# Kernel optimization log

Hardware: AMD Instinct MI355X
Metric: run time of the kernel (lower is better)

## Reference

```python
import jax, jax.numpy as jnp
import numpy as np

GAMMA = 0.1      # L1 weight
N_STEPS = 10     # inner ISTA/RMSProp iterations
RHO = 0.9        # RMSProp decay
LR = 0.001
MOMENTUM = 0.9
EPS = 1e-8       # RMSProp epsilon
ABS_EPS = 1e-6   # smooth-abs epsilon (seya diff_abs)


def setup_inputs() -> dict:
    key = jax.random.key(0)
    k1, k2 = jax.random.split(key)
    B, D_in, D_out = 32768, 128, 512
    inputs = jax.random.normal(k1, (B, D_in), dtype=jnp.float32)
    # glorot_uniform for W of shape (output_dim, input_dim)
    limit = float(np.sqrt(6.0 / (D_out + D_in)))
    W = jax.random.uniform(k2, (D_out, D_in), jnp.float32, -limit, limit)
    return {"inputs": inputs, "W": W}


def _grad_x(x, W, inputs):
    # cost = sum((inputs - x @ W)^2) + gamma * sum(sqrt(x^2 + ABS_EPS))
    recon = x @ W                        # [B, D_in]
    g = 2.0 * ((recon - inputs) @ W.T)   # analytic d(rec_error)/dx, [B, D_out]
    g = g + GAMMA * x / jnp.sqrt(x * x + ABS_EPS)  # d(smooth L1)/dx
    return g


def reference(inputs, W):
    B = inputs.shape[0]
    D_out = W.shape[0]
    x0 = jnp.zeros((B, D_out), inputs.dtype)
    a1_0 = jnp.zeros_like(x0)
    a2_0 = jnp.zeros_like(x0)

    def step(carry, _):
        x, a1, a2 = carry
        g = _grad_x(x, W, inputs)
        new_a1 = RHO * a1 + (1.0 - RHO) * g * g
        upd = LR * g / jnp.sqrt(new_a1 + EPS)
        new_a2 = MOMENTUM * a2 - upd
        new_x = x + MOMENTUM * new_a2 - upd
        return (new_x, new_a1, new_a2), None

    (xT, _, _), _ = jax.lax.scan(step, (x0, a1_0, a2_0), None, length=N_STEPS)
    return xT  # final sparse codes [B, D_out] (return_reconstruction=False)
```

## Files before the change

kernel.cpp:

```cpp
#include <hip/hip_runtime.h>


#define BSZ   32768
#define DIN   128
#define DOUT  512
#define RTILE 16
#define NSTEP 10
#define NBLOCKS (BSZ / RTILE)

__global__ void sc_pack(const float* __restrict__ W, float* __restrict__ W4,
                        float* __restrict__ Wt4) {
    const int tid = blockIdx.x * blockDim.x + threadIdx.x;
    const int j = tid >> 7;
    const int i = tid & 127;
    const float v = W[j * DIN + i];
    W4 [(j >> 2) * 512  + i * 4 + (j & 3)] = v;
    Wt4[(i >> 2) * 2048 + j * 4 + (i & 3)] = v;
}

__global__ __launch_bounds__(256, 4)
void sc_fused(const float* __restrict__ inp, const float4* __restrict__ W4,
              const float4* __restrict__ Wt4, float* __restrict__ out)
{
    __shared__ float x_lds[RTILE][DOUT];
    __shared__ float d_lds[RTILE][DIN];

    const int t = threadIdx.x;
    const int row0 = blockIdx.x * RTILE;

    const int i_p1 = t & 127;
    const int rg   = (t >> 7) * 8;
    const int j0   = 2 * t;

    float a1[RTILE][2];
    float a2[RTILE][2];
#pragma unroll
    for (int r = 0; r < RTILE; ++r) {
        a1[r][0] = a1[r][1] = 0.f;
        a2[r][0] = a2[r][1] = 0.f;
    }

    float inr[8];
#pragma unroll
    for (int rr = 0; rr < 8; ++rr)
        inr[rr] = inp[(row0 + rg + rr) * DIN + i_p1];

    for (int k = t; k < RTILE * DOUT; k += 256) (&x_lds[0][0])[k] = 0.f;
    __syncthreads();

    const float4* __restrict__ w4p  = W4 + i_p1;
    const float4* __restrict__ wt4p = Wt4 + j0;

    for (int step = 0; step < NSTEP; ++step) {
        {
            float acc[8];
#pragma unroll
            for (int rr = 0; rr < 8; ++rr) acc[rr] = 0.f;

#pragma unroll 2
            for (int jb = 0; jb < DOUT / 4; ++jb) {
                const float4 wv = w4p[jb * 128];
#pragma unroll
                for (int rr = 0; rr < 8; ++rr) {
                    const float4 xv = *(const float4*)&x_lds[rg + rr][jb * 4];
                    acc[rr] = fmaf(xv.x, wv.x, acc[rr]);
                    acc[rr] = fmaf(xv.y, wv.y, acc[rr]);
                    acc[rr] = fmaf(xv.z, wv.z, acc[rr]);
                    acc[rr] = fmaf(xv.w, wv.w, acc[rr]);
                }
            }
#pragma unroll
            for (int rr = 0; rr < 8; ++rr)
                d_lds[rg + rr][i_p1] = acc[rr] - inr[rr];
        }
        __syncthreads();

        {
            float acc[RTILE][2];
#pragma unroll
            for (int r = 0; r < RTILE; ++r) acc[r][0] = acc[r][1] = 0.f;

#pragma unroll 2
            for (int ib = 0; ib < DIN / 4; ++ib) {
                const float4 wqa = wt4p[ib * 512];
                const float4 wqb = wt4p[ib * 512 + 1];
#pragma unroll
                for (int r = 0; r < RTILE; ++r) {
                    const float4 dv = *(const float4*)&d_lds[r][ib * 4];
                    acc[r][0] = fmaf(dv.x, wqa.x, acc[r][0]);
                    acc[r][0] = fmaf(dv.y, wqa.y, acc[r][0]);
                    acc[r][0] = fmaf(dv.z, wqa.z, acc[r][0]);
                    acc[r][0] = fmaf(dv.w, wqa.w, acc[r][0]);
                    acc[r][1] = fmaf(dv.x, wqb.x, acc[r][1]);
                    acc[r][1] = fmaf(dv.y, wqb.y, acc[r][1]);
                    acc[r][1] = fmaf(dv.z, wqb.z, acc[r][1]);
                    acc[r][1] = fmaf(dv.w, wqb.w, acc[r][1]);
                }
            }

#pragma unroll
            for (int r = 0; r < RTILE; ++r) {
#pragma unroll
                for (int c = 0; c < 2; ++c) {
                    const float xv  = x_lds[r][j0 + c];
                    const float g   = 2.f * acc[r][c] + 0.1f * xv * rsqrtf(xv * xv + 1e-6f);
                    const float na1 = 0.9f * a1[r][c] + 0.1f * g * g;
                    a1[r][c] = na1;
                    const float upd = 0.001f * g * rsqrtf(na1 + 1e-8f);
                    const float na2 = 0.9f * a2[r][c] - upd;
                    a2[r][c] = na2;
                    x_lds[r][j0 + c] = xv + 0.9f * na2 - upd;
                }
            }
            __syncthreads();
        }
    }

    for (int k = t; k < RTILE * DOUT; k += 256)
        out[row0 * DOUT + k] = (&x_lds[0][0])[k];
}

extern "C" void kernel_launch(void* const* d_in, const int* in_sizes, int n_in,
                              void* d_out, int out_size, void* d_ws, size_t ws_size,
                              hipStream_t stream) {
    const float* inputs = (const float*)d_in[0];
    const float* W      = (const float*)d_in[1];
    float* out          = (float*)d_out;
    float* W4           = (float*)d_ws;
    float* Wt4          = (float*)d_ws + 65536;

    sc_pack<<<dim3(256), dim3(256), 0, stream>>>(W, W4, Wt4);
    sc_fused<<<dim3(NBLOCKS), dim3(256), 0, stream>>>(inputs, (const float4*)W4,
                                                      (const float4*)Wt4, out);
}
```

Before: 1.641 ms.

## Double threads per block, keep x in registers, skip zero first matmul

Raises the block to 512 threads so each thread owns one output column and four rows in the first product instead of two columns and eight rows. The optimizer state x is now held in registers as well as LDS, which removes the LDS reads of x in the update. The first step skips the x@W product because x starts at zero, which also drops the LDS zero-init loop. The cost is more waves per block and a changed occupancy target through launch bounds (512, 6). Each thread also issues narrower weight loads per FMA, so there is less work per load.

New measurement: 1.974 ms. 1.2x slower.

```diff
diff --git a/kernel.cpp b/kernel.cpp
--- a/kernel.cpp
+++ b/kernel.cpp
@@ -6,6 +6,7 @@
 #define DOUT  512
 #define RTILE 16
 #define NSTEP 10
+#define NT    512
 #define NBLOCKS (BSZ / RTILE)
 
 __global__ void sc_pack(const float* __restrict__ W, float* __restrict__ W4,
@@ -18,7 +19,7 @@
     Wt4[(i >> 2) * 2048 + j * 4 + (i & 3)] = v;
 }
 
-__global__ __launch_bounds__(256, 4)
+__global__ __launch_bounds__(NT, 6)
 void sc_fused(const float* __restrict__ inp, const float4* __restrict__ W4,
               const float4* __restrict__ Wt4, float* __restrict__ out)
 {
@@ -29,39 +30,36 @@
     const int row0 = blockIdx.x * RTILE;
 
     const int i_p1 = t & 127;
-    const int rg   = (t >> 7) * 8;
-    const int j0   = 2 * t;
+    const int rg   = (t >> 7) * 4;
+    const int j0   = t;
 
-    float a1[RTILE][2];
-    float a2[RTILE][2];
+    float xs[RTILE], a1[RTILE], a2[RTILE];
 #pragma unroll
-    for (int r = 0; r < RTILE; ++r) {
-        a1[r][0] = a1[r][1] = 0.f;
-        a2[r][0] = a2[r][1] = 0.f;
-    }
+    for (int r = 0; r < RTILE; ++r) { xs[r] = 0.f; a1[r] = 0.f; a2[r] = 0.f; }
 
-    float inr[8];
+    float inr[4];
 #pragma unroll
-    for (int rr = 0; rr < 8; ++rr)
+    for (int rr = 0; rr < 4; ++rr)
         inr[rr] = inp[(row0 + rg + rr) * DIN + i_p1];
-
-    for (int k = t; k < RTILE * DOUT; k += 256) (&x_lds[0][0])[k] = 0.f;
-    __syncthreads();
 
     const float4* __restrict__ w4p  = W4 + i_p1;
     const float4* __restrict__ wt4p = Wt4 + j0;
 
     for (int step = 0; step < NSTEP; ++step) {
-        {
-            float acc[8];
+        if (step == 0) {
 #pragma unroll
-            for (int rr = 0; rr < 8; ++rr) acc[rr] = 0.f;
+            for (int rr = 0; rr < 4; ++rr)
+                d_lds[rg + rr][i_p1] = 0.0f - inr[rr];
+        } else {
+            float acc[4];
+#pragma unroll
+            for (int rr = 0; rr < 4; ++rr) acc[rr] = 0.f;
 
 #pragma unroll 2
             for (int jb = 0; jb < DOUT / 4; ++jb) {
                 const float4 wv = w4p[jb * 128];
 #pragma unroll
-                for (int rr = 0; rr < 8; ++rr) {
+                for (int rr = 0; rr < 4; ++rr) {
                     const float4 xv = *(const float4*)&x_lds[rg + rr][jb * 4];
                     acc[rr] = fmaf(xv.x, wv.x, acc[rr]);
                     acc[rr] = fmaf(xv.y, wv.y, acc[rr]);
@@ -70,53 +68,47 @@
                 }
             }
 #pragma unroll
-            for (int rr = 0; rr < 8; ++rr)
+            for (int rr = 0; rr < 4; ++rr)
                 d_lds[rg + rr][i_p1] = acc[rr] - inr[rr];
         }
         __syncthreads();
 
         {
-            float acc[RTILE][2];
+            float acc2[RTILE];
 #pragma unroll
-            for (int r = 0; r < RTILE; ++r) acc[r][0] = acc[r][1] = 0.f;
+            for (int r = 0; r < RTILE; ++r) acc2[r] = 0.f;
 
 #pragma unroll 2
             for (int ib = 0; ib < DIN / 4; ++ib) {
-                const float4 wqa = wt4p[ib * 512];
-                const float4 wqb = wt4p[ib * 512 + 1];
+                const float4 wq = wt4p[ib * 512];
 #pragma unroll
                 for (int r = 0; r < RTILE; ++r) {
                     const float4 dv = *(const float4*)&d_lds[r][ib * 4];
-                    acc[r][0] = fmaf(dv.x, wqa.x, acc[r][0]);
-                    acc[r][0] = fmaf(dv.y, wqa.y, acc[r][0]);
-                    acc[r][0] = fmaf(dv.z, wqa.z, acc[r][0]);
-                    acc[r][0] = fmaf(dv.w, wqa.w, acc[r][0]);
-                    acc[r][1] = fmaf(dv.x, wqb.x, acc[r][1]);
-                    acc[r][1] = fmaf(dv.y, wqb.y, acc[r][1]);
-                    acc[r][1] = fmaf(dv.z, wqb.z, acc[r][1]);
-                    acc[r][1] = fmaf(dv.w, wqb.w, acc[r][1]);
+                    acc2[r] = fmaf(dv.x, wq.x, acc2[r]);
+                    acc2[r] = fmaf(dv.y, wq.y, acc2[r]);
+                    acc2[r] = fmaf(dv.z, wq.z, acc2[r]);
+                    acc2[r] = fmaf(dv.w, wq.w, acc2[r]);
                 }
             }
 
 #pragma unroll
             for (int r = 0; r < RTILE; ++r) {
-#pragma unroll
-                for (int c = 0; c < 2; ++c) {
-                    const float xv  = x_lds[r][j0 + c];
-                    const float g   = 2.f * acc[r][c] + 0.1f * xv * rsqrtf(xv * xv + 1e-6f);
-                    const float na1 = 0.9f * a1[r][c] + 0.1f * g * g;
-                    a1[r][c] = na1;
-                    const float upd = 0.001f * g * rsqrtf(na1 + 1e-8f);
-                    const float na2 = 0.9f * a2[r][c] - upd;
-                    a2[r][c] = na2;
-                    x_lds[r][j0 + c] = xv + 0.9f * na2 - upd;
-                }
+                const float xv  = xs[r];
+                const float g   = 2.f * acc2[r] + 0.1f * xv * rsqrtf(xv * xv + 1e-6f);
+                const float na1 = 0.9f * a1[r] + 0.1f * g * g;
+                a1[r] = na1;
+                const float upd = 0.001f * g * rsqrtf(na1 + 1e-8f);
+                const float na2 = 0.9f * a2[r] - upd;
+                a2[r] = na2;
+                const float xn = xv + 0.9f * na2 - upd;
+                xs[r] = xn;
+                x_lds[r][j0] = xn;
             }
             __syncthreads();
         }
     }
 
-    for (int k = t; k < RTILE * DOUT; k += 256)
+    for (int k = t; k < RTILE * DOUT; k += NT)
         out[row0 * DOUT + k] = (&x_lds[0][0])[k];
 }
 
@@ -130,6 +122,6 @@
     float* Wt4          = (float*)d_ws + 65536;
 
     sc_pack<<<dim3(256), dim3(256), 0, stream>>>(W, W4, Wt4);
-    sc_fused<<<dim3(NBLOCKS), dim3(256), 0, stream>>>(inputs, (const float4*)W4,
-                                                      (const float4*)Wt4, out);
+    sc_fused<<<dim3(NBLOCKS), dim3(NT), 0, stream>>>(inputs, (const float4*)W4,
+                                                     (const float4*)Wt4, out);
 }
```

## Retile first GEMM to 4x2 per thread, skip zero-x step, stage inputs in LDS

Applied to the files above, without the earlier changes.

The first matmul (x@W) is remapped so each thread computes 4 rows by 2 input columns instead of 8 rows by 1 column. This halves LDS reads of x per FMA at the cost of two global W loads per iteration. The first step skips the x@W product because x is zero. Inputs are now staged in shared memory instead of registers, the x_lds zero-init is dropped, and launch bounds are lowered from 4 to 3 waves per SIMD, which gives more registers but may reduce occupancy.

Result: slower. 1.798 ms (+9.6%).

```diff
diff --git a/kernel.cpp b/kernel.cpp
--- a/kernel.cpp
+++ b/kernel.cpp
@@ -6,6 +6,7 @@
 #define DOUT  512
 #define RTILE 16
 #define NSTEP 10
+#define NT    256
 #define NBLOCKS (BSZ / RTILE)
 
 __global__ void sc_pack(const float* __restrict__ W, float* __restrict__ W4,
@@ -18,19 +19,20 @@
     Wt4[(i >> 2) * 2048 + j * 4 + (i & 3)] = v;
 }
 
-__global__ __launch_bounds__(256, 4)
+__global__ __launch_bounds__(NT, 3)
 void sc_fused(const float* __restrict__ inp, const float4* __restrict__ W4,
               const float4* __restrict__ Wt4, float* __restrict__ out)
 {
     __shared__ float x_lds[RTILE][DOUT];
     __shared__ float d_lds[RTILE][DIN];
+    __shared__ float inp_lds[RTILE][DIN];
 
     const int t = threadIdx.x;
     const int row0 = blockIdx.x * RTILE;
 
-    const int i_p1 = t & 127;
-    const int rg   = (t >> 7) * 8;
-    const int j0   = 2 * t;
+    const int ic = (t & 63) * 2;
+    const int rg = (t >> 6) * 4;
+    const int j0 = 2 * t;
 
     float a1[RTILE][2];
     float a2[RTILE][2];
@@ -40,61 +42,71 @@
         a2[r][0] = a2[r][1] = 0.f;
     }
 
-    float inr[8];
-#pragma unroll
-    for (int rr = 0; rr < 8; ++rr)
-        inr[rr] = inp[(row0 + rg + rr) * DIN + i_p1];
-
-    for (int k = t; k < RTILE * DOUT; k += 256) (&x_lds[0][0])[k] = 0.f;
+    for (int k = t; k < RTILE * DIN; k += NT)
+        (&inp_lds[0][0])[k] = inp[row0 * DIN + k];
     __syncthreads();
 
-    const float4* __restrict__ w4p  = W4 + i_p1;
+    const float4* __restrict__ w4a  = W4 + ic;
+    const float4* __restrict__ w4b  = W4 + ic + 1;
     const float4* __restrict__ wt4p = Wt4 + j0;
 
     for (int step = 0; step < NSTEP; ++step) {
-        {
-            float acc[8];
+        if (step == 0) {
 #pragma unroll
-            for (int rr = 0; rr < 8; ++rr) acc[rr] = 0.f;
+            for (int rr = 0; rr < 4; ++rr) {
+                d_lds[rg + rr][ic + 0] = 0.0f - inp_lds[rg + rr][ic + 0];
+                d_lds[rg + rr][ic + 1] = 0.0f - inp_lds[rg + rr][ic + 1];
+            }
+        } else {
+            float acc[4][2];
+#pragma unroll
+            for (int rr = 0; rr < 4; ++rr) acc[rr][0] = acc[rr][1] = 0.f;
 
 #pragma unroll 2
             for (int jb = 0; jb < DOUT / 4; ++jb) {
-                const float4 wv = w4p[jb * 128];
+                const float4 wa = w4a[jb * 128];
+                const float4 wb = w4b[jb * 128];
 #pragma unroll
-                for (int rr = 0; rr < 8; ++rr) {
+                for (int rr = 0; rr < 4; ++rr) {
                     const float4 xv = *(const float4*)&x_lds[rg + rr][jb * 4];
-                    acc[rr] = fmaf(xv.x, wv.x, acc[rr]);
-                    acc[rr] = fmaf(xv.y, wv.y, acc[rr]);
-                    acc[rr] = fmaf(xv.z, wv.z, acc[rr]);
-                    acc[rr] = fmaf(xv.w, wv.w, acc[rr]);
+                    acc[rr][0] = fmaf(xv.x, wa.x, acc[rr][0]);
+                    acc[rr][0] = fmaf(xv.y, wa.y, acc[rr][0]);
+                    acc[rr][0] = fmaf(xv.z, wa.z, acc[rr][0]);
+                    acc[rr][0] = fmaf(xv.w, wa.w, acc[rr][0]);
+                    acc[rr][1] = fmaf(xv.x, wb.x, acc[rr][1]);
+                    acc[rr][1] = fmaf(xv.y, wb.y, acc[rr][1]);
+                    acc[rr][1] = fmaf(xv.z, wb.z, acc[rr][1]);
+                    acc[rr][1] = fmaf(xv.w, wb.w, acc[rr][1]);
                 }
             }
 #pragma unroll
-            for (int rr = 0; rr < 8; ++rr)
-                d_lds[rg + rr][i_p1] = acc[rr] - inr[rr];
+            for (int rr = 0; rr < 4; ++rr) {
+                d_lds[rg + rr][ic + 0] = acc[rr][0] - inp_lds[rg + rr][ic + 0];
+                d_lds[rg + rr][ic + 1] = acc[rr][1] - inp_lds[rg + rr][ic + 1];
+            }
         }
         __syncthreads();
 
         {
-            float acc[RTILE][2];
+            float acc2[RTILE][2];
 #pragma unroll
-            for (int r = 0; r < RTILE; ++r) acc[r][0] = acc[r][1] = 0.f;
+            for (int r = 0; r < RTILE; ++r) acc2[r][0] = acc2[r][1] = 0.f;
 
 #pragma unroll 2
             for (int ib = 0; ib < DIN / 4; ++ib) {
-                const float4 wqa = wt4p[ib * 512];
-                const float4 wqb = wt4p[ib * 512 + 1];
+                const float4 qa = wt4p[ib * 512];
+                const float4 qb = wt4p[ib * 512 + 1];
 #pragma unroll
                 for (int r = 0; r < RTILE; ++r) {
                     const float4 dv = *(const float4*)&d_lds[r][ib * 4];
-                    acc[r][0] = fmaf(dv.x, wqa.x, acc[r][0]);
-                    acc[r][0] = fmaf(dv.y, wqa.y, acc[r][0]);
-                    acc[r][0] = fmaf(dv.z, wqa.z, acc[r][0]);
-                    acc[r][0] = fmaf(dv.w, wqa.w, acc[r][0]);
-                    acc[r][1] = fmaf(dv.x, wqb.x, acc[r][1]);
-                    acc[r][1] = fmaf(dv.y, wqb.y, acc[r][1]);
-                    acc[r][1] = fmaf(dv.z, wqb.z, acc[r][1]);
-                    acc[r][1] = fmaf(dv.w, wqb.w, acc[r][1]);
+                    acc2[r][0] = fmaf(dv.x, qa.x, acc2[r][0]);
+                    acc2[r][0] = fmaf(dv.y, qa.y, acc2[r][0]);
+                    acc2[r][0] = fmaf(dv.z, qa.z, acc2[r][0]);
+                    acc2[r][0] = fmaf(dv.w, qa.w, acc2[r][0]);
+                    acc2[r][1] = fmaf(dv.x, qb.x, acc2[r][1]);
+                    acc2[r][1] = fmaf(dv.y, qb.y, acc2[r][1]);
+                    acc2[r][1] = fmaf(dv.z, qb.z, acc2[r][1]);
+                    acc2[r][1] = fmaf(dv.w, qb.w, acc2[r][1]);
                 }
             }
 
@@ -102,8 +114,8 @@
             for (int r = 0; r < RTILE; ++r) {
 #pragma unroll
                 for (int c = 0; c < 2; ++c) {
-                    const float xv  = x_lds[r][j0 + c];
-                    const float g   = 2.f * acc[r][c] + 0.1f * xv * rsqrtf(xv * xv + 1e-6f);
+                    const float xv  = (step == 0) ? 0.0f : x_lds[r][j0 + c];
+                    const float g   = 2.f * acc2[r][c] + 0.1f * xv * rsqrtf(xv * xv + 1e-6f);
                     const float na1 = 0.9f * a1[r][c] + 0.1f * g * g;
                     a1[r][c] = na1;
                     const float upd = 0.001f * g * rsqrtf(na1 + 1e-8f);
@@ -116,7 +128,7 @@
         }
     }
 
-    for (int k = t; k < RTILE * DOUT; k += 256)
+    for (int k = t; k < RTILE * DOUT; k += NT)
         out[row0 * DOUT + k] = (&x_lds[0][0])[k];
 }
 
@@ -130,6 +142,6 @@
     float* Wt4          = (float*)d_ws + 65536;
 
     sc_pack<<<dim3(256), dim3(256), 0, stream>>>(W, W4, Wt4);
-    sc_fused<<<dim3(NBLOCKS), dim3(256), 0, stream>>>(inputs, (const float4*)W4,
-                                                      (const float4*)Wt4, out);
+    sc_fused<<<dim3(NBLOCKS), dim3(NT), 0, stream>>>(inputs, (const float4*)W4,
+                                                     (const float4*)Wt4, out);
 }
```
